# Performance work log

Hardware: AMD Instinct MI355X
Metric: run time of the kernel (lower is better)

Reference implementation:

```python
import jax, jax.numpy as jnp
import numpy as np
import math

B, Hdim, Wdim = 8, 32, 32
CH = [64, 128, 256, 512]
KV = 960


def setup_inputs() -> dict:
    key = jax.random.key(0)
    ks = jax.random.split(key, 24)
    f32 = jnp.float32
    inp = {}
    inp["emb1"] = jax.random.normal(ks[0], (B, CH[0], Hdim, Wdim), f32)
    inp["emb2"] = jax.random.normal(ks[1], (B, CH[1], Hdim, Wdim), f32)
    inp["emb3"] = jax.random.normal(ks[2], (B, CH[2], Hdim, Wdim), f32)
    inp["emb4"] = jax.random.normal(ks[3], (B, CH[3], Hdim, Wdim), f32)
    inp["emb_all"] = jax.random.normal(ks[4], (B, KV, Hdim, Wdim), f32)
    s = 0.05  # small init so softmax/instnorm stay well-conditioned
    inp["w_mhead1"] = jax.random.normal(ks[5], (CH[0], CH[0]), f32) * s
    inp["w_mhead2"] = jax.random.normal(ks[6], (CH[1], CH[1]), f32) * s
    inp["w_mhead3"] = jax.random.normal(ks[7], (CH[2], CH[2]), f32) * s
    inp["w_mhead4"] = jax.random.normal(ks[8], (CH[3], CH[3]), f32) * s
    inp["w_mheadq"] = jax.random.normal(ks[9], (KV, KV), f32) * s
    inp["w_mheadk"] = jax.random.normal(ks[10], (KV, KV), f32) * s
    inp["w_mheadv"] = jax.random.normal(ks[11], (KV, KV), f32) * s
    inp["w_q1"] = jax.random.normal(ks[12], (CH[0], 2, 3, 3), f32) * s
    inp["w_q2"] = jax.random.normal(ks[13], (CH[1], 2, 3, 3), f32) * s
    inp["w_q3"] = jax.random.normal(ks[14], (CH[2], 2, 3, 3), f32) * s
    inp["w_q4"] = jax.random.normal(ks[15], (CH[3], 2, 3, 3), f32) * s
    inp["w_qc"] = jax.random.normal(ks[16], (KV, 1, 3, 3), f32) * s
    inp["w_kc"] = jax.random.normal(ks[17], (KV, 1, 3, 3), f32) * s
    inp["w_vc"] = jax.random.normal(ks[18], (KV, 1, 3, 3), f32) * s
    inp["w_proj1"] = jax.random.normal(ks[19], (CH[0], CH[0]), f32) * s
    inp["w_proj2"] = jax.random.normal(ks[20], (CH[1], CH[1]), f32) * s
    inp["w_proj3"] = jax.random.normal(ks[21], (CH[2], CH[2]), f32) * s
    inp["w_proj4"] = jax.random.normal(ks[22], (CH[3], CH[3]), f32) * s
    return inp


def conv1x1(x, w):
    # x: [b,c,h,w], w: [o,c] (1x1 conv, no bias)
    return jnp.einsum('bchw,oc->bohw', x, w)


def dwconv3x3(x, w, groups):
    # torch grouped conv: w [O, C//g, 3, 3]
    return jax.lax.conv_general_dilated(
        x, w, window_strides=(1, 1), padding='SAME',
        dimension_numbers=('NCHW', 'OIHW', 'NCHW'),
        feature_group_count=groups)


def l2norm(x):
    # F.normalize(dim=-1): divide by max(||x||_2, 1e-12)
    n = jnp.sqrt(jnp.sum(x * x, axis=-1, keepdims=True))
    return x / jnp.maximum(n, 1e-12)


def instnorm(x, eps=1e-5):
    # InstanceNorm2d(head=1, affine=False) on [b, head, c, n]: normalize per (b, head)
    m = jnp.mean(x, axis=(2, 3), keepdims=True)
    v = jnp.var(x, axis=(2, 3), keepdims=True)
    return (x - m) * jax.lax.rsqrt(v + eps)


def reference(emb1, emb2, emb3, emb4, emb_all,
              w_mhead1, w_mhead2, w_mhead3, w_mhead4,
              w_mheadq, w_mheadk, w_mheadv,
              w_q1, w_q2, w_q3, w_q4,
              w_qc, w_kc, w_vc,
              w_proj1, w_proj2, w_proj3, w_proj4):
    b, _, h, w = emb1.shape
    hw = h * w
    scale = 1.0 / math.sqrt(KV)

    # channel cross-attention over the concatenated features
    Qc = dwconv3x3(conv1x1(emb_all, w_mheadq), w_qc, KV).reshape(b, 1, KV, hw)
    Kc = dwconv3x3(conv1x1(emb_all, w_mheadk), w_kc, KV).reshape(b, 1, KV, hw)
    Vc = dwconv3x3(conv1x1(emb_all, w_mheadv), w_vc, KV).reshape(b, 1, KV, hw)
    Qc = l2norm(Qc)
    Kc = l2norm(Kc)
    sim = jnp.einsum('bhcn,bhdn->bhcd', Qc, Kc) * scale  # [b,1,KV,KV]
    sim = jax.nn.softmax(instnorm(sim), axis=-1)
    ctx = jnp.einsum('bhcd,bhdn->bhcn', sim, Vc)  # [b,1,KV,hw]

    def branch(emb, w_mh, w_q, groups, w_proj):
        c = emb.shape[1]
        q = dwconv3x3(conv1x1(emb, w_mh), w_q, groups).reshape(b, 1, c, hw)
        q = l2norm(q)
        attn = jnp.einsum('bhcn,bhdn->bhcd', q, ctx) * scale  # [b,1,c,KV]
        p = jax.nn.softmax(instnorm(attn), axis=-1)
        o = jnp.einsum('bhcd,bhdn->bhcn', p, ctx)  # [b,1,c,hw]
        o = jnp.mean(o, axis=1).reshape(b, c, h, w)
        return conv1x1(o, w_proj)

    O1 = branch(emb1, w_mhead1, w_q1, CH[0] // 2, w_proj1)
    O2 = branch(emb2, w_mhead2, w_q2, CH[1] // 2, w_proj2)
    O3 = branch(emb3, w_mhead3, w_q3, CH[2] // 2, w_proj3)
    O4 = branch(emb4, w_mhead4, w_q4, CH[3] // 2, w_proj4)
    return (O1, O2, O3, O4)
```

## Files before the change

kernel.cpp:

```cpp
#include <hip/hip_runtime.h>
#include <hip/hip_bf16.h>
#include <math.h>

#define NB 8
#define HWN 1024
#define KVC 960

typedef short bf16x8 __attribute__((ext_vector_type(8)));
typedef float f32x4 __attribute__((ext_vector_type(4)));
typedef unsigned short ushort_t;

__device__ inline ushort_t f2bf(float f) {
    __hip_bfloat16 h = __float2bfloat16(f);
    return *reinterpret_cast<ushort_t*>(&h);
}
__device__ inline float bf2f(ushort_t u) {
    union { float f; unsigned int i; } x; x.i = ((unsigned int)u) << 16; return x.f;
}
__device__ inline void glds16(const ushort_t* src, ushort_t* dst) {
    __builtin_amdgcn_global_load_lds(
        (const __attribute__((address_space(1))) void*)src,
        (__attribute__((address_space(3))) void*)dst, 16, 0, 0);
}

struct F2BTab {
    const float* src[12];
    long dstOff[12];
    int nblk[12];
    int nseg;
};

__global__ __launch_bounds__(256)
void f2b_batched(F2BTab tab, ushort_t* base)
{
    int b = blockIdx.x, s = 0;
    while (s < tab.nseg - 1 && b >= tab.nblk[s]) { b -= tab.nblk[s]; ++s; }
    float4 v = *((const float4*)tab.src[s] + (long)b * 256 + threadIdx.x);
    ushort4 o = make_ushort4(f2bf(v.x), f2bf(v.y), f2bf(v.z), f2bf(v.w));
    *((ushort4*)(base + tab.dstOff[s]) + (long)b * 256 + threadIdx.x) = o;
}

struct F2TTab {
    const float* src[5];
    long dstOff[5];
    long sIn[5], sOut[5];
    int R[5];
    int nblk[5];
    int nseg;
};

__global__ __launch_bounds__(256)
void f2bt_batched(F2TTab tab, ushort_t* base)
{
    __shared__ ushort_t tile[64][65];
    int b = blockIdx.x, s = 0;
    while (s < tab.nseg - 1 && b >= tab.nblk[s]) { b -= tab.nblk[s]; ++s; }
    const int R = tab.R[s];
    const int tpb = (R >> 6) * 16;
    const int batch = b / tpb, rem = b - batch * tpb;
    const int rtile = rem >> 4, ctile = rem & 15;
    const float* ib = tab.src[s] + (long)batch * tab.sIn[s] + (long)(rtile * 64) * 1024 + ctile * 64;
    const int t = threadIdx.x, tr = t >> 4, tc = (t & 15) * 4;
    #pragma unroll
    for (int p = 0; p < 4; ++p) {
        float4 v = *(const float4*)(ib + (long)(tr + 16 * p) * 1024 + tc);
        tile[tr + 16 * p][tc + 0] = f2bf(v.x);
        tile[tr + 16 * p][tc + 1] = f2bf(v.y);
        tile[tr + 16 * p][tc + 2] = f2bf(v.z);
        tile[tr + 16 * p][tc + 3] = f2bf(v.w);
    }
    __syncthreads();
    ushort_t* ob = base + tab.dstOff[s] + (long)batch * tab.sOut[s]
                 + (long)(ctile * 64) * R + rtile * 64;
    #pragma unroll
    for (int p = 0; p < 4; ++p) {
        ushort4 v;
        v.x = tile[tc + 0][tr + 16 * p];
        v.y = tile[tc + 1][tr + 16 * p];
        v.z = tile[tc + 2][tr + 16 * p];
        v.w = tile[tc + 3][tr + 16 * p];
        *(ushort4*)(ob + (long)(tr + 16 * p) * R + tc) = v;
    }
}

__global__ __launch_bounds__(256)
void trb_kernel(const ushort_t* __restrict__ in, ushort_t* __restrict__ out)
{
    __shared__ ushort_t tile[64][65];
    const int r0 = blockIdx.y * 64, c0 = blockIdx.x * 64;
    const long sP = (long)KVC * HWN;
    const ushort_t* ib = in + (long)blockIdx.z * sP;
    ushort_t* ob = out + (long)blockIdx.z * sP;
    const int t = threadIdx.x, tr = t >> 4, tc = (t & 15) * 4;
    #pragma unroll
    for (int p = 0; p < 4; ++p) {
        ushort4 v = *(const ushort4*)(ib + (long)(r0 + tr + 16 * p) * 1024 + c0 + tc);
        tile[tr + 16 * p][tc + 0] = v.x;
        tile[tr + 16 * p][tc + 1] = v.y;
        tile[tr + 16 * p][tc + 2] = v.z;
        tile[tr + 16 * p][tc + 3] = v.w;
    }
    __syncthreads();
    #pragma unroll
    for (int p = 0; p < 4; ++p) {
        ushort4 v;
        v.x = tile[tc + 0][tr + 16 * p];
        v.y = tile[tc + 1][tr + 16 * p];
        v.z = tile[tc + 2][tr + 16 * p];
        v.w = tile[tc + 3][tr + 16 * p];
        *(ushort4*)(ob + (long)(c0 + tr + 16 * p) * 960 + r0 + tc) = v;
    }
}

__global__ __launch_bounds__(256)
void mfma_gemm_nt_stats(const ushort_t* __restrict__ A, const ushort_t* __restrict__ B,
                        float* __restrict__ C, float2* __restrict__ part,
                        int M, int N, int K, long sA, long sB, long sC, float alpha)
{
    __shared__ __align__(16) ushort_t lA[128 * 64];
    __shared__ __align__(16) ushort_t lB[128 * 64];
    const int bb = blockIdx.x;
    const int by = blockIdx.y, bx = blockIdx.z;
    const ushort_t* Ab = A + (long)bb * sA;
    const ushort_t* Bb = B + (long)bb * sB;
    const int row0 = by * 128, col0 = bx * 128;
    const int t = threadIdx.x, lane = t & 63, w = t >> 6;
    const int wr = w >> 1, wc = w & 1;
    const int arl = lane >> 3;
    const int acs = ((lane & 7) ^ arl) * 8;
    int arow[4], brow[4];
    #pragma unroll
    for (int j = 0; j < 4; ++j) {
        int r = row0 + w * 32 + j * 8 + arl;  arow[j] = r < M ? r : M - 1;
        int rb = col0 + w * 32 + j * 8 + arl; brow[j] = rb < N ? rb : N - 1;
    }

    f32x4 acc[4][4];
    #pragma unroll
    for (int m = 0; m < 4; ++m)
        #pragma unroll
        for (int n = 0; n < 4; ++n)
            acc[m][n] = (f32x4){0.f, 0.f, 0.f, 0.f};

    for (int k0 = 0; k0 < K; k0 += 64) {
        #pragma unroll
        for (int j = 0; j < 4; ++j) {
            glds16(Ab + (long)arow[j] * K + k0 + acs, lA + (w * 32 + j * 8) * 64);
            glds16(Bb + (long)brow[j] * K + k0 + acs, lB + (w * 32 + j * 8) * 64);
        }
        __syncthreads();
        #pragma unroll
        for (int sub = 0; sub < 2; ++sub) {
            const int kc = (lane >> 4) + sub * 4;
            bf16x8 aF[4], bF[4];
            #pragma unroll
            for (int m = 0; m < 4; ++m) {
                int rl = wr * 64 + m * 16 + (lane & 15);
                aF[m] = *(const bf16x8*)(lA + rl * 64 + (kc ^ (rl & 7)) * 8);
            }
            #pragma unroll
            for (int n = 0; n < 4; ++n) {
                int rl = wc * 64 + n * 16 + (lane & 15);
                bF[n] = *(const bf16x8*)(lB + rl * 64 + (kc ^ (rl & 7)) * 8);
            }
            #pragma unroll
            for (int m = 0; m < 4; ++m)
                #pragma unroll
                for (int n = 0; n < 4; ++n)
                    acc[m][n] = __builtin_amdgcn_mfma_f32_16x16x32_bf16(aF[m], bF[n], acc[m][n], 0, 0, 0);
        }
        __syncthreads();
    }

    const int cr0 = row0 + wr * 64 + (lane >> 4) * 4;
    const int cc0 = col0 + wc * 64 + (lane & 15);
    float* Cb = C + (long)bb * sC;
    float s1 = 0.f, s2 = 0.f;
    #pragma unroll
    for (int m = 0; m < 4; ++m) {
        #pragma unroll
        for (int n = 0; n < 4; ++n) {
            int ccol = cc0 + n * 16;
            if (ccol >= N) continue;
            #pragma unroll
            for (int r = 0; r < 4; ++r) {
                int crow = cr0 + m * 16 + r;
                if (crow < M) {
                    float v = acc[m][n][r] * alpha;
                    Cb[(long)crow * N + ccol] = v;
                    s1 += v; s2 += v * v;
                }
            }
        }
    }
    #pragma unroll
    for (int off = 32; off > 0; off >>= 1) {
        s1 += __shfl_down(s1, off);
        s2 += __shfl_down(s2, off);
    }
    float* rbuf = (float*)lA;
    if (lane == 0) { rbuf[w] = s1; rbuf[4 + w] = s2; }
    __syncthreads();
    if (t == 0)
        part[(bb * 8 + by) * 8 + bx] =
            make_float2(rbuf[0] + rbuf[1] + rbuf[2] + rbuf[3],
                        rbuf[4] + rbuf[5] + rbuf[6] + rbuf[7]);
}

struct NTTab {
    const ushort_t* A[5];
    const ushort_t* B[5];
    void* C[5];
    long sA[5], sB[5], sC[5], ldb[5];
    int M[5], K[5], obf[5], mt0[5];
    int nseg;
};

__global__ __launch_bounds__(256)
void mfma_gemm_nt_tab(NTTab tab)
{
    __shared__ __align__(16) ushort_t lA[128 * 64];
    __shared__ __align__(16) ushort_t lB[128 * 64];
    const int bb = blockIdx.x;
    int si = 0;
    #pragma unroll
    for (int s = 1; s < 5; ++s)
        if (s < tab.nseg && (int)blockIdx.y >= tab.mt0[s]) si = s;
    const int M = tab.M[si], K = tab.K[si];
    const long ldb = tab.ldb[si];
    const ushort_t* Ab = tab.A[si] + (long)bb * tab.sA[si];
    const ushort_t* Bb = tab.B[si] + (long)bb * tab.sB[si];
    const int row0 = (blockIdx.y - tab.mt0[si]) * 128, col0 = blockIdx.z * 128;
    const int t = threadIdx.x, lane = t & 63, w = t >> 6;
    const int wr = w >> 1, wc = w & 1;
    const int arl = lane >> 3;
    const int acs = ((lane & 7) ^ arl) * 8;
    int arow[4], brow[4];
    #pragma unroll
    for (int j = 0; j < 4; ++j) {
        int r = row0 + w * 32 + j * 8 + arl;
        arow[j] = r < M ? r : M - 1;
        brow[j] = col0 + w * 32 + j * 8 + arl;
    }

    f32x4 acc[4][4];
    #pragma unroll
    for (int m = 0; m < 4; ++m)
        #pragma unroll
        for (int n = 0; n < 4; ++n)
            acc[m][n] = (f32x4){0.f, 0.f, 0.f, 0.f};

    for (int k0 = 0; k0 < K; k0 += 64) {
        #pragma unroll
        for (int j = 0; j < 4; ++j) {
            glds16(Ab + (long)arow[j] * K + k0 + acs, lA + (w * 32 + j * 8) * 64);
            glds16(Bb + (long)brow[j] * ldb + k0 + acs, lB + (w * 32 + j * 8) * 64);
        }
        __syncthreads();
        #pragma unroll
        for (int sub = 0; sub < 2; ++sub) {
            const int kc = (lane >> 4) + sub * 4;
            bf16x8 aF[4], bF[4];
            #pragma unroll
            for (int m = 0; m < 4; ++m) {
                int rl = wr * 64 + m * 16 + (lane & 15);
                aF[m] = *(const bf16x8*)(lA + rl * 64 + (kc ^ (rl & 7)) * 8);
            }
            #pragma unroll
            for (int n = 0; n < 4; ++n) {
                int rl = wc * 64 + n * 16 + (lane & 15);
                bF[n] = *(const bf16x8*)(lB + rl * 64 + (kc ^ (rl & 7)) * 8);
            }
            #pragma unroll
            for (int m = 0; m < 4; ++m)
                #pragma unroll
                for (int n = 0; n < 4; ++n)
                    acc[m][n] = __builtin_amdgcn_mfma_f32_16x16x32_bf16(aF[m], bF[n], acc[m][n], 0, 0, 0);
        }
        __syncthreads();
    }

    const int cr0 = row0 + wr * 64 + (lane >> 4) * 4;
    const int cc0 = col0 + wc * 64 + (lane & 15);
    const int obf = tab.obf[si];
    ushort_t* Cb_b = (ushort_t*)tab.C[si] + (long)bb * tab.sC[si];
    float* Cb_f = (float*)tab.C[si] + (long)bb * tab.sC[si];
    #pragma unroll
    for (int m = 0; m < 4; ++m) {
        #pragma unroll
        for (int n = 0; n < 4; ++n) {
            int ccol = cc0 + n * 16;
            #pragma unroll
            for (int r = 0; r < 4; ++r) {
                int crow = cr0 + m * 16 + r;
                if (crow < M) {
                    float v = acc[m][n][r];
                    if (obf) Cb_b[(long)crow * 1024 + ccol] = f2bf(v);
                    else     Cb_f[(long)crow * 1024 + ccol] = v;
                }
            }
        }
    }
}

__global__ __launch_bounds__(256)
void stencil_all(const ushort_t* __restrict__ Xqkv, const ushort_t* __restrict__ mh_x,
                 const float* __restrict__ w_qc, const float* __restrict__ w_kc,
                 const float* __restrict__ w_vc,
                 const float* __restrict__ wq1, const float* __restrict__ wq2,
                 const float* __restrict__ wq3, const float* __restrict__ wq4,
                 ushort_t* __restrict__ Qc, ushort_t* __restrict__ Kc,
                 ushort_t* __restrict__ Vc, ushort_t* __restrict__ q_all)
{
    __shared__ float p0[32 * 33];
    __shared__ float p1[32 * 33];
    __shared__ float red[5];
    const int bid = blockIdx.x;
    const int t = threadIdx.x;
    const int i0 = t * 4, y = i0 >> 5, x0 = i0 & 31;

    if (bid < 23040) {
        const int which = bid / 7680;
        const int p = bid - which * 7680;
        const int b = p / 960, c = p - b * 960;
        const ushort_t* ip = Xqkv + ((long)b * 2880 + which * 960 + c) * 1024;
        const float* wgt = (which == 0 ? w_qc : which == 1 ? w_kc : w_vc) + c * 9;
        ushort_t* op = (which == 0 ? Qc : which == 1 ? Kc : Vc) + (long)p * 1024;
        ushort4 u = *(const ushort4*)(ip + i0);
        float* rw = p0 + y * 33 + x0;
        rw[0] = bf2f(u.x); rw[1] = bf2f(u.y); rw[2] = bf2f(u.z); rw[3] = bf2f(u.w);
        __syncthreads();
        float W[9];
        #pragma unroll
        for (int q = 0; q < 9; ++q) W[q] = wgt[q];
        float r[3][6];
        #pragma unroll
        for (int dy = 0; dy < 3; ++dy) {
            int yy = y + dy - 1;
            bool vy = (unsigned)yy < 32u;
            #pragma unroll
            for (int j = 0; j < 6; ++j) {
                int xx = x0 - 1 + j;
                r[dy][j] = (vy && (unsigned)xx < 32u) ? p0[yy * 33 + xx] : 0.f;
            }
        }
        float o[4];
        #pragma unroll
        for (int q = 0; q < 4; ++q)
            o[q] = r[0][q] * W[0] + r[0][q + 1] * W[1] + r[0][q + 2] * W[2]
                 + r[1][q] * W[3] + r[1][q + 1] * W[4] + r[1][q + 2] * W[5]
                 + r[2][q] * W[6] + r[2][q + 1] * W[7] + r[2][q + 2] * W[8];
        float inv = 1.f;
        if (which < 2) {
            float s = o[0] * o[0] + o[1] * o[1] + o[2] * o[2] + o[3] * o[3];
            #pragma unroll
            for (int off = 32; off > 0; off >>= 1) s += __shfl_down(s, off);
            if ((t & 63) == 0) red[t >> 6] = s;
            __syncthreads();
            if (t == 0) red[4] = 1.0f / fmaxf(sqrtf(red[0] + red[1] + red[2] + red[3]), 1e-12f);
            __syncthreads();
            inv = red[4];
        }
        *(ushort4*)(op + i0) =
            make_ushort4(f2bf(o[0] * inv), f2bf(o[1] * inv), f2bf(o[2] * inv), f2bf(o[3] * inv));
        return;
    }
    const int po = bid - 23040;
    const int o = po & 1023, b = po >> 10;
    ushort_t* op = q_all + (long)po * 1024;
    int off; const float* wbase;
    if (o < 64)       { off = 0;   wbase = wq1; }
    else if (o < 128) { *(ushort4*)(op + i0) = make_ushort4(0, 0, 0, 0); return; }
    else if (o < 256) { off = 128; wbase = wq2; }
    else if (o < 512) { off = 256; wbase = wq3; }
    else              { off = 512; wbase = wq4; }
    const int ol = o - off;
    const int g2 = ol & ~1;
    const ushort_t* ip0 = mh_x + ((long)(b << 10) + off + g2) * 1024;
    const ushort_t* ip1 = ip0 + 1024;
    ushort4 u0 = *(const ushort4*)(ip0 + i0);
    ushort4 u1 = *(const ushort4*)(ip1 + i0);
    float* r0w = p0 + y * 33 + x0;
    float* r1w = p1 + y * 33 + x0;
    r0w[0] = bf2f(u0.x); r0w[1] = bf2f(u0.y); r0w[2] = bf2f(u0.z); r0w[3] = bf2f(u0.w);
    r1w[0] = bf2f(u1.x); r1w[1] = bf2f(u1.y); r1w[2] = bf2f(u1.z); r1w[3] = bf2f(u1.w);
    __syncthreads();
    const float* wp = wbase + ol * 18;
    float W[18];
    #pragma unroll
    for (int q = 0; q < 18; ++q) W[q] = wp[q];
    float o4[4] = {0.f, 0.f, 0.f, 0.f};
    #pragma unroll
    for (int pl = 0; pl < 2; ++pl) {
        const float* src = pl ? p1 : p0;
        const float* Wp = W + pl * 9;
        float r[3][6];
        #pragma unroll
        for (int dy = 0; dy < 3; ++dy) {
            int yy = y + dy - 1;
            bool vy = (unsigned)yy < 32u;
            #pragma unroll
            for (int j = 0; j < 6; ++j) {
                int xx = x0 - 1 + j;
                r[dy][j] = (vy && (unsigned)xx < 32u) ? src[yy * 33 + xx] : 0.f;
            }
        }
        #pragma unroll
        for (int q = 0; q < 4; ++q)
            o4[q] += r[0][q] * Wp[0] + r[0][q + 1] * Wp[1] + r[0][q + 2] * Wp[2]
                   + r[1][q] * Wp[3] + r[1][q + 1] * Wp[4] + r[1][q + 2] * Wp[5]
                   + r[2][q] * Wp[6] + r[2][q + 1] * Wp[7] + r[2][q + 2] * Wp[8];
    }
    float s = o4[0] * o4[0] + o4[1] * o4[1] + o4[2] * o4[2] + o4[3] * o4[3];
    #pragma unroll
    for (int off2 = 32; off2 > 0; off2 >>= 1) s += __shfl_down(s, off2);
    if ((t & 63) == 0) red[t >> 6] = s;
    __syncthreads();
    if (t == 0) red[4] = 1.0f / fmaxf(sqrtf(red[0] + red[1] + red[2] + red[3]), 1e-12f);
    __syncthreads();
    float inv = red[4];
    *(ushort4*)(op + i0) =
        make_ushort4(f2bf(o4[0] * inv), f2bf(o4[1] * inv), f2bf(o4[2] * inv), f2bf(o4[3] * inv));
}

__global__ void reduce_sim(const float2* __restrict__ part, float2* __restrict__ stats)
{
    float2 p = part[blockIdx.x * 64 + threadIdx.x];
    float s1 = p.x, s2 = p.y;
    #pragma unroll
    for (int off = 32; off > 0; off >>= 1) {
        s1 += __shfl_down(s1, off);
        s2 += __shfl_down(s2, off);
    }
    if (threadIdx.x == 0) stats[blockIdx.x] = make_float2(s1, s2);
}

__global__ void reduce_branch(const float2* __restrict__ part, float2* __restrict__ stats)
{
    const int br = blockIdx.x & 3, b = blockIdx.x >> 2;
    const int lo4[4] = {0, 1, 2, 4}, hi4[4] = {1, 2, 4, 8};
    float s1 = 0.f, s2 = 0.f;
    if (threadIdx.x < 8) {
        for (int my = lo4[br]; my < hi4[br]; ++my) {
            float2 p = part[(b * 8 + my) * 8 + threadIdx.x];
            s1 += p.x; s2 += p.y;
        }
    }
    #pragma unroll
    for (int off = 32; off > 0; off >>= 1) {
        s1 += __shfl_down(s1, off);
        s2 += __shfl_down(s2, off);
    }
    if (threadIdx.x == 0) stats[b * 4 + br] = make_float2(s1, s2);
}

__global__ __launch_bounds__(256)
void instnorm_softmax_bf16(const float* __restrict__ x, ushort_t* __restrict__ out,
                           const float2* __restrict__ stats, int rowsPerB, float invL)
{
    int row = blockIdx.x;
    int b = row / rowsPerB;
    float2 st = stats[b];
    float mean = st.x * invL;
    float var = st.y * invL - mean * mean;
    float rinv = rsqrtf(var + 1e-5f);
    const float* xr = x + (long)row * 960;
    ushort_t* orow = out + (long)row * 960;
    int t = threadIdx.x;
    float v[4];
    float mx = -1e30f;
    #pragma unroll
    for (int q = 0; q < 4; ++q) {
        int i = t + q * 256;
        if (i < 960) { v[q] = (xr[i] - mean) * rinv; mx = fmaxf(mx, v[q]); }
        else v[q] = -1e30f;
    }
    #pragma unroll
    for (int off = 32; off > 0; off >>= 1) mx = fmaxf(mx, __shfl_down(mx, off));
    __shared__ float rm[4];
    __shared__ float bmax, bsuminv;
    if ((t & 63) == 0) rm[t >> 6] = mx;
    __syncthreads();
    if (t == 0) bmax = fmaxf(fmaxf(rm[0], rm[1]), fmaxf(rm[2], rm[3]));
    __syncthreads();
    float mall = bmax;
    float s = 0.f;
    #pragma unroll
    for (int q = 0; q < 4; ++q) {
        int i = t + q * 256;
        if (i < 960) { v[q] = __expf(v[q] - mall); s += v[q]; }
    }
    #pragma unroll
    for (int off = 32; off > 0; off >>= 1) s += __shfl_down(s, off);
    if ((t & 63) == 0) rm[t >> 6] = s;
    __syncthreads();
    if (t == 0) bsuminv = 1.0f / (rm[0] + rm[1] + rm[2] + rm[3]);
    __syncthreads();
    float invS = bsuminv;
    #pragma unroll
    for (int q = 0; q < 4; ++q) {
        int i = t + q * 256;
        if (i < 960) orow[i] = f2bf(v[q] * invS);
    }
}

__global__ __launch_bounds__(256)
void softmax_attn_kernel(const float* __restrict__ x, ushort_t* __restrict__ P,
                         const float2* __restrict__ stats)
{
    const int r = blockIdx.x & 1023, b = blockIdx.x >> 10;
    const int t = threadIdx.x;
    ushort_t* orow = P + ((long)(b << 10) + r) * 960;
    int br; float cnt;
    if (r < 64)       { br = 0; cnt = 64.f; }
    else if (r < 128) {
        #pragma unroll
        for (int q = 0; q < 4; ++q) {
            int i = t + q * 256;
            if (i < 960) orow[i] = 0;
        }
        return;
    }
    else if (r < 256) { br = 1; cnt = 128.f; }
    else if (r < 512) { br = 2; cnt = 256.f; }
    else              { br = 3; cnt = 512.f; }
    float invL = 1.0f / (cnt * 960.f);
    float2 st = stats[b * 4 + br];
    float mean = st.x * invL;
    float var = st.y * invL - mean * mean;
    float rinv = rsqrtf(var + 1e-5f);
    const float* xr = x + ((long)(b << 10) + r) * 960;
    float v[4];
    float mx = -1e30f;
    #pragma unroll
    for (int q = 0; q < 4; ++q) {
        int i = t + q * 256;
        if (i < 960) { v[q] = (xr[i] - mean) * rinv; mx = fmaxf(mx, v[q]); }
        else v[q] = -1e30f;
    }
    #pragma unroll
    for (int off = 32; off > 0; off >>= 1) mx = fmaxf(mx, __shfl_down(mx, off));
    __shared__ float rm[4];
    __shared__ float bmax, bsuminv;
    if ((t & 63) == 0) rm[t >> 6] = mx;
    __syncthreads();
    if (t == 0) bmax = fmaxf(fmaxf(rm[0], rm[1]), fmaxf(rm[2], rm[3]));
    __syncthreads();
    float mall = bmax;
    float s = 0.f;
    #pragma unroll
    for (int q = 0; q < 4; ++q) {
        int i = t + q * 256;
        if (i < 960) { v[q] = __expf(v[q] - mall); s += v[q]; }
    }
    #pragma unroll
    for (int off = 32; off > 0; off >>= 1) s += __shfl_down(s, off);
    if ((t & 63) == 0) rm[t >> 6] = s;
    __syncthreads();
    if (t == 0) bsuminv = 1.0f / (rm[0] + rm[1] + rm[2] + rm[3]);
    __syncthreads();
    float invS = bsuminv;
    #pragma unroll
    for (int q = 0; q < 4; ++q) {
        int i = t + q * 256;
        if (i < 960) orow[i] = f2bf(v[q] * invS);
    }
}


extern "C" void kernel_launch(void* const* d_in, const int* in_sizes, int n_in,
                              void* d_out, int out_size, void* d_ws, size_t ws_size,
                              hipStream_t stream)
{
    const float* emb[4]  = {(const float*)d_in[0], (const float*)d_in[1],
                            (const float*)d_in[2], (const float*)d_in[3]};
    const float* emb_all = (const float*)d_in[4];
    const float* w_mh[4] = {(const float*)d_in[5], (const float*)d_in[6],
                            (const float*)d_in[7], (const float*)d_in[8]};
    const float* w_mq = (const float*)d_in[9];
    const float* w_mk = (const float*)d_in[10];
    const float* w_mv = (const float*)d_in[11];
    const float* w_q[4] = {(const float*)d_in[12], (const float*)d_in[13],
                           (const float*)d_in[14], (const float*)d_in[15]};
    const float* w_qc = (const float*)d_in[16];
    const float* w_kc = (const float*)d_in[17];
    const float* w_vc = (const float*)d_in[18];
    const float* w_proj[4] = {(const float*)d_in[19], (const float*)d_in[20],
                              (const float*)d_in[21], (const float*)d_in[22]};
    float* out = (float*)d_out;

    ushort_t* U = (ushort_t*)d_ws;
    const long eWQKV = 0;
    const long eWMH  = 2764800;
    const long eWPJ  = 3112960;
    const long eR1   = 3461120;
    const long eR2   = 11325440;
    const long eR3   = 19189760;
    const long ePc   = 34918400;
    const long eR4   = 42782720;
    const long eQc   = 51171328;
    const long eKc   = 59035648;
    const long eQall = 66899968;
    float2* part  = (float2*)(U + 75288576);
    float2* stats = part + 512;

    ushort_t* WQKVb = U + eWQKV;
    ushort_t* WMHb  = U + eWMH;
    ushort_t* WPJb  = U + eWPJ;
    ushort_t* embT_all = U + eR1;
    ushort_t* Vc    = U + eR1;
    ushort_t* ctx   = U + eR1;
    ushort_t* VcT   = U + eR2;
    ushort_t* ctxT  = U + eR2;
    ushort_t* Xqkv  = U + eR3;
    float*    S6    = (float*)(U + eR3);
    ushort_t* oT    = U + eR3;
    ushort_t* Pc    = U + ePc;
    ushort_t* mh_x  = U + eR4;
    ushort_t* P_all = U + eR4;
    ushort_t* QcB   = U + eQc;
    ushort_t* KcB   = U + eKc;
    ushort_t* q_all = U + eQall;
    ushort_t* embT_i[4] = {U + eR2, U + eR2 + 524288, U + eR2 + 1572864, U + eR2 + 3670016};

    const float scale = 0.0322748612183951400f;
    const long SB = (long)KVC * HWN;
    const long S1024 = 1024L * 1024;
    const int CH[4] = {64, 128, 256, 512};
    const int mhoff[4] = {0, 4096, 20480, 86016};
    const int rowOff[4] = {0, 128, 256, 512};
    const long outOff[4] = {0, 524288, 1572864, 3670016};
    dim3 blk(256);

    {
        F2BTab tf;
        const float* fs[11] = {w_mq, w_mk, w_mv, w_mh[0], w_mh[1], w_mh[2], w_mh[3],
                               w_proj[0], w_proj[1], w_proj[2], w_proj[3]};
        long fd[11] = {eWQKV, eWQKV + 921600, eWQKV + 1843200,
                       eWMH + 0, eWMH + 4096, eWMH + 20480, eWMH + 86016,
                       eWPJ + 0, eWPJ + 4096, eWPJ + 20480, eWPJ + 86016};
        int fn[11] = {900, 900, 900, 4, 16, 64, 256, 4, 16, 64, 256};
        int ftot = 0;
        for (int i = 0; i < 11; ++i) { tf.src[i] = fs[i]; tf.dstOff[i] = fd[i]; tf.nblk[i] = fn[i]; ftot += fn[i]; }
        tf.nseg = 11;
        f2b_batched<<<ftot, blk, 0, stream>>>(tf, U);
    }
    {
        F2TTab tt;
        const float* ts[5] = {emb_all, emb[0], emb[1], emb[2], emb[3]};
        long td[5] = {eR1, eR2, eR2 + 524288, eR2 + 1572864, eR2 + 3670016};
        int tR[5] = {960, 64, 128, 256, 512};
        int tn[5];
        long tsi[5], tso[5];
        int ttot = 0;
        for (int i = 0; i < 5; ++i) {
            tsi[i] = (long)tR[i] * 1024; tso[i] = tsi[i];
            tn[i] = NB * (tR[i] / 64) * 16; ttot += tn[i];
            tt.src[i] = ts[i]; tt.dstOff[i] = td[i]; tt.R[i] = tR[i];
            tt.sIn[i] = tsi[i]; tt.sOut[i] = tso[i]; tt.nblk[i] = tn[i];
        }
        tt.nseg = 5;
        f2bt_batched<<<ttot, blk, 0, stream>>>(tt, U);
    }

    auto nt1 = [&](const ushort_t* A, long sA, const ushort_t* B, long sB, long ldb,
                   void* C, long sC, int M, int K, int obf) {
        NTTab tb;
        for (int s = 0; s < 5; ++s) {
            tb.A[s] = A; tb.B[s] = B; tb.C[s] = C;
            tb.sA[s] = sA; tb.sB[s] = sB; tb.sC[s] = sC; tb.ldb[s] = ldb;
            tb.M[s] = M; tb.K[s] = K; tb.obf[s] = obf; tb.mt0[s] = (s == 0) ? 0 : (1 << 30);
        }
        tb.nseg = 1;
        dim3 g(NB, (M + 127) / 128, 8);
        mfma_gemm_nt_tab<<<g, blk, 0, stream>>>(tb);
    };

    {
        NTTab tb;
        tb.A[0] = WQKVb; tb.B[0] = embT_all; tb.C[0] = Xqkv;
        tb.sA[0] = 0; tb.sB[0] = SB; tb.sC[0] = 2880L * 1024; tb.ldb[0] = 960;
        tb.M[0] = 2880; tb.K[0] = 960; tb.obf[0] = 1; tb.mt0[0] = 0;
        int mt = 23;
        for (int i = 0; i < 4; ++i) {
            tb.A[1 + i] = WMHb + mhoff[i]; tb.B[1 + i] = embT_i[i];
            tb.C[1 + i] = mh_x + (long)rowOff[i] * 1024;
            tb.sA[1 + i] = 0; tb.sB[1 + i] = (long)CH[i] * 1024; tb.sC[1 + i] = S1024;
            tb.ldb[1 + i] = CH[i];
            tb.M[1 + i] = CH[i]; tb.K[1 + i] = CH[i]; tb.obf[1 + i] = 1; tb.mt0[1 + i] = mt;
            mt += (CH[i] + 127) / 128;
        }
        tb.nseg = 5;
        dim3 g(NB, mt, 8);
        mfma_gemm_nt_tab<<<g, blk, 0, stream>>>(tb);
    }

    stencil_all<<<31232, blk, 0, stream>>>(Xqkv, mh_x, w_qc, w_kc, w_vc,
                                           w_q[0], w_q[1], w_q[2], w_q[3],
                                           QcB, KcB, Vc, q_all);

    trb_kernel<<<dim3(16, 15, NB), blk, 0, stream>>>(Vc, VcT);

    mfma_gemm_nt_stats<<<dim3(NB, 8, 8), blk, 0, stream>>>(
        QcB, KcB, S6, part, KVC, KVC, HWN, SB, SB, (long)KVC * KVC, scale);
    reduce_sim<<<NB, 64, 0, stream>>>(part, stats);
    instnorm_softmax_bf16<<<NB * KVC, blk, 0, stream>>>(S6, Pc, stats, KVC,
                                                        1.f / ((float)KVC * (float)KVC));

    nt1(Pc, (long)KVC * KVC, VcT, SB, 960, ctx, SB, KVC, KVC, 1);

    trb_kernel<<<dim3(16, 15, NB), blk, 0, stream>>>(ctx, ctxT);

    mfma_gemm_nt_stats<<<dim3(NB, 8, 8), blk, 0, stream>>>(
        q_all, ctx, S6, part, 1024, KVC, HWN, S1024, SB, SB, scale);
    reduce_branch<<<32, 64, 0, stream>>>(part, stats);
    softmax_attn_kernel<<<NB * 1024, blk, 0, stream>>>(S6, P_all, stats);

    nt1(ctxT, SB, P_all, SB, 960, oT, S1024, 1024, KVC, 1);

    {
        NTTab tb;
        int mt = 0;
        for (int i = 0; i < 4; ++i) {
            tb.A[i] = WPJb + mhoff[i]; tb.B[i] = oT + rowOff[i];
            tb.C[i] = out + outOff[i];
            tb.sA[i] = 0; tb.sB[i] = S1024; tb.sC[i] = (long)CH[i] * 1024;
            tb.ldb[i] = 1024;
            tb.M[i] = CH[i]; tb.K[i] = CH[i]; tb.obf[i] = 0; tb.mt0[i] = mt;
            mt += (CH[i] + 127) / 128;
        }
        tb.A[4] = tb.A[3]; tb.B[4] = tb.B[3]; tb.C[4] = tb.C[3];
        tb.sA[4] = 0; tb.sB[4] = 0; tb.sC[4] = 0; tb.ldb[4] = 1024;
        tb.M[4] = 1; tb.K[4] = 64; tb.obf[4] = 0; tb.mt0[4] = 1 << 30;
        tb.nseg = 4;
        dim3 g(NB, mt, 8);
        mfma_gemm_nt_tab<<<g, blk, 0, stream>>>(tb);
    }

    (void)in_sizes; (void)n_in; (void)out_size; (void)ws_size;
}
```

Baseline: 320.5 us.

## Double-buffer LDS tiles in MFMA NT GEMMs to overlap loads with compute

Both the stats GEMM and the table-driven NT GEMM now keep two LDS buffers. Each iteration issues the global-to-LDS loads for the next K tile, then waits on a partial vmcnt before computing on the current tile, so memory latency overlaps with MFMA work. s_setprio raises wave priority around the compute phase. LDS use per block doubles, which may lower occupancy, and the hand-written waitcnt and barrier ordering is fragile.

```diff
diff --git a/kernel.cpp b/kernel.cpp
--- a/kernel.cpp
+++ b/kernel.cpp
@@ -117,8 +117,8 @@
                         float* __restrict__ C, float2* __restrict__ part,
                         int M, int N, int K, long sA, long sB, long sC, float alpha)
 {
-    __shared__ __align__(16) ushort_t lA[128 * 64];
-    __shared__ __align__(16) ushort_t lB[128 * 64];
+    __shared__ __align__(16) ushort_t lA[2][128 * 64];
+    __shared__ __align__(16) ushort_t lB[2][128 * 64];
     const int bb = blockIdx.x;
     const int by = blockIdx.y, bx = blockIdx.z;
     const ushort_t* Ab = A + (long)bb * sA;
@@ -142,13 +142,15 @@
         for (int n = 0; n < 4; ++n)
             acc[m][n] = (f32x4){0.f, 0.f, 0.f, 0.f};
 
-    for (int k0 = 0; k0 < K; k0 += 64) {
+    auto stage = [&](int buf, int k0) {
         #pragma unroll
         for (int j = 0; j < 4; ++j) {
-            glds16(Ab + (long)arow[j] * K + k0 + acs, lA + (w * 32 + j * 8) * 64);
-            glds16(Bb + (long)brow[j] * K + k0 + acs, lB + (w * 32 + j * 8) * 64);
-        }
-        __syncthreads();
+            glds16(Ab + (long)arow[j] * K + k0 + acs, lA[buf] + (w * 32 + j * 8) * 64);
+            glds16(Bb + (long)brow[j] * K + k0 + acs, lB[buf] + (w * 32 + j * 8) * 64);
+        }
+    };
+    auto compute = [&](int buf) {
+        __builtin_amdgcn_s_setprio(1);
         #pragma unroll
         for (int sub = 0; sub < 2; ++sub) {
             const int kc = (lane >> 4) + sub * 4;
@@ -156,12 +158,12 @@
             #pragma unroll
             for (int m = 0; m < 4; ++m) {
                 int rl = wr * 64 + m * 16 + (lane & 15);
-                aF[m] = *(const bf16x8*)(lA + rl * 64 + (kc ^ (rl & 7)) * 8);
+                aF[m] = *(const bf16x8*)(lA[buf] + rl * 64 + (kc ^ (rl & 7)) * 8);
             }
             #pragma unroll
             for (int n = 0; n < 4; ++n) {
                 int rl = wc * 64 + n * 16 + (lane & 15);
-                bF[n] = *(const bf16x8*)(lB + rl * 64 + (kc ^ (rl & 7)) * 8);
+                bF[n] = *(const bf16x8*)(lB[buf] + rl * 64 + (kc ^ (rl & 7)) * 8);
             }
             #pragma unroll
             for (int m = 0; m < 4; ++m)
@@ -169,8 +171,24 @@
                 for (int n = 0; n < 4; ++n)
                     acc[m][n] = __builtin_amdgcn_mfma_f32_16x16x32_bf16(aF[m], bF[n], acc[m][n], 0, 0, 0);
         }
-        __syncthreads();
-    }
+        __builtin_amdgcn_s_setprio(0);
+    };
+
+    stage(0, 0);
+    int cur = 0;
+    for (int k0 = 64; k0 < K; k0 += 64) {
+        stage(cur ^ 1, k0);
+        asm volatile("s_waitcnt vmcnt(8)" ::: "memory");
+        __builtin_amdgcn_sched_barrier(0);
+        __builtin_amdgcn_s_barrier();
+        compute(cur);
+        __builtin_amdgcn_s_barrier();
+        cur ^= 1;
+    }
+    asm volatile("s_waitcnt vmcnt(0)" ::: "memory");
+    __builtin_amdgcn_sched_barrier(0);
+    __builtin_amdgcn_s_barrier();
+    compute(cur);
 
     const int cr0 = row0 + wr * 64 + (lane >> 4) * 4;
     const int cc0 = col0 + wc * 64 + (lane & 15);
@@ -198,6 +216,7 @@
         s1 += __shfl_down(s1, off);
         s2 += __shfl_down(s2, off);
     }
+    __syncthreads();
     float* rbuf = (float*)lA;
     if (lane == 0) { rbuf[w] = s1; rbuf[4 + w] = s2; }
     __syncthreads();
@@ -219,8 +238,8 @@
 __global__ __launch_bounds__(256)
 void mfma_gemm_nt_tab(NTTab tab)
 {
-    __shared__ __align__(16) ushort_t lA[128 * 64];
-    __shared__ __align__(16) ushort_t lB[128 * 64];
+    __shared__ __align__(16) ushort_t lA[2][128 * 64];
+    __shared__ __align__(16) ushort_t lB[2][128 * 64];
     const int bb = blockIdx.x;
     int si = 0;
     #pragma unroll
@@ -250,13 +269,15 @@
         for (int n = 0; n < 4; ++n)
             acc[m][n] = (f32x4){0.f, 0.f, 0.f, 0.f};
 
-    for (int k0 = 0; k0 < K; k0 += 64) {
+    auto stage = [&](int buf, int k0) {
         #pragma unroll
         for (int j = 0; j < 4; ++j) {
-            glds16(Ab + (long)arow[j] * K + k0 + acs, lA + (w * 32 + j * 8) * 64);
-            glds16(Bb + (long)brow[j] * ldb + k0 + acs, lB + (w * 32 + j * 8) * 64);
-        }
-        __syncthreads();
+            glds16(Ab + (long)arow[j] * K + k0 + acs, lA[buf] + (w * 32 + j * 8) * 64);
+            glds16(Bb + (long)brow[j] * ldb + k0 + acs, lB[buf] + (w * 32 + j * 8) * 64);
+        }
+    };
+    auto compute = [&](int buf) {
+        __builtin_amdgcn_s_setprio(1);
         #pragma unroll
         for (int sub = 0; sub < 2; ++sub) {
             const int kc = (lane >> 4) + sub * 4;
@@ -264,12 +285,12 @@
             #pragma unroll
             for (int m = 0; m < 4; ++m) {
                 int rl = wr * 64 + m * 16 + (lane & 15);
-                aF[m] = *(const bf16x8*)(lA + rl * 64 + (kc ^ (rl & 7)) * 8);
+                aF[m] = *(const bf16x8*)(lA[buf] + rl * 64 + (kc ^ (rl & 7)) * 8);
             }
             #pragma unroll
             for (int n = 0; n < 4; ++n) {
                 int rl = wc * 64 + n * 16 + (lane & 15);
-                bF[n] = *(const bf16x8*)(lB + rl * 64 + (kc ^ (rl & 7)) * 8);
+                bF[n] = *(const bf16x8*)(lB[buf] + rl * 64 + (kc ^ (rl & 7)) * 8);
             }
             #pragma unroll
             for (int m = 0; m < 4; ++m)
@@ -277,8 +298,24 @@
                 for (int n = 0; n < 4; ++n)
                     acc[m][n] = __builtin_amdgcn_mfma_f32_16x16x32_bf16(aF[m], bF[n], acc[m][n], 0, 0, 0);
         }
-        __syncthreads();
-    }
+        __builtin_amdgcn_s_setprio(0);
+    };
+
+    stage(0, 0);
+    int cur = 0;
+    for (int k0 = 64; k0 < K; k0 += 64) {
+        stage(cur ^ 1, k0);
+        asm volatile("s_waitcnt vmcnt(8)" ::: "memory");
+        __builtin_amdgcn_sched_barrier(0);
+        __builtin_amdgcn_s_barrier();
+        compute(cur);
+        __builtin_amdgcn_s_barrier();
+        cur ^= 1;
+    }
+    asm volatile("s_waitcnt vmcnt(0)" ::: "memory");
+    __builtin_amdgcn_sched_barrier(0);
+    __builtin_amdgcn_s_barrier();
+    compute(cur);
 
     const int cr0 = row0 + wr * 64 + (lane >> 4) * 4;
     const int cc0 = col0 + wc * 64 + (lane & 15);
```

After: 303.8 us. 5.2% less time.
